# Kernel tuning notes

Hardware: AMD Instinct MI355X
Metric: run time of the kernel (lower is better)

Reference implementation:

```python
import jax, jax.numpy as jnp
import numpy as np

N_FEAT = 27  # 26 embeddings + bot MLP output
LI = np.array([i for i in range(N_FEAT) for j in range(i)])
LJ = np.array([j for i in range(N_FEAT) for j in range(i)])


def _mlp(x, Ws, bs):
    for W, b in zip(Ws, bs):
        x = jax.nn.relu(x @ W + b)
    return x


def setup_inputs() -> dict:
    key = jax.random.key(0)
    ks = jax.random.split(key, 32)
    B, V, D = 32768, 50000, 128
    bot = [13, 512, 256, 128]
    top = [479, 1024, 1024, 512, 256, 1]
    inp = {
        "dense_x": jax.random.normal(ks[0], (B, 13), dtype=jnp.float32),
        "sparse_x": jax.random.randint(ks[1], (B, 26), 0, V, dtype=jnp.int64),
        "emb": jax.random.normal(ks[2], (26, V, D), dtype=jnp.float32) * 0.01,
    }
    for i in range(3):
        inp[f"bw{i}"] = jax.random.normal(ks[3 + i], (bot[i], bot[i + 1]), dtype=jnp.float32) * (1.0 / np.sqrt(bot[i]))
        inp[f"bb{i}"] = jnp.zeros((bot[i + 1],), dtype=jnp.float32)
    for i in range(5):
        inp[f"tw{i}"] = jax.random.normal(ks[8 + i], (top[i], top[i + 1]), dtype=jnp.float32) * (1.0 / np.sqrt(top[i]))
        inp[f"tb{i}"] = jnp.zeros((top[i + 1],), dtype=jnp.float32)
    return inp


def reference(dense_x, sparse_x, emb,
              bw0, bb0, bw1, bb1, bw2, bb2,
              tw0, tb0, tw1, tb1, tw2, tb2, tw3, tb3, tw4, tb4):
    B = dense_x.shape[0]
    bot_out = _mlp(dense_x, [bw0, bw1, bw2], [bb0, bb1, bb2])  # [B, 128]
    # multi-table embedding gather: emb[t, sparse_x[:, t]] -> [B, 26, 128]
    gathered = jnp.take_along_axis(
        emb[None, :, :, :],  # broadcast over batch via vmap-style gather
        sparse_x.T[None, :, :, None].astype(jnp.int32) * 0, 0
    ) if False else jnp.stack(
        [emb[t][sparse_x[:, t]] for t in range(emb.shape[0])], axis=1
    )
    features = jnp.concatenate([bot_out[:, None, :], gathered], axis=1)  # [B, 27, 128]
    # batched dot interaction: [B, 27, 27], then triangular gather
    Z = jnp.einsum('bnd,bmd->bnm', features, features)
    interact = Z[:, LI, LJ]  # [B, 351]
    x = jnp.concatenate([bot_out, interact], axis=1)  # [B, 479]
    return _mlp(x, [tw0, tw1, tw2, tw3, tw4], [tb0, tb1, tb2, tb3, tb4])  # [B, 1]
```

## Files before the change

### kernel.cpp

```cpp
#include <hip/hip_runtime.h>

typedef _Float16 f16;
typedef __attribute__((ext_vector_type(2))) _Float16 f16x2;
typedef __attribute__((ext_vector_type(4))) _Float16 f16x4;
typedef __attribute__((ext_vector_type(8))) _Float16 f16x8;
typedef __attribute__((ext_vector_type(4))) float f32x4;

#define BM 128
#define BN 128
#define BK 32

#define TBM 256
#define TBN 256
#define TBK 64

__device__ __forceinline__ void gl_lds16(const void* g, void* l) {
    __builtin_amdgcn_global_load_lds(
        (const __attribute__((address_space(1))) void*)g,
        (__attribute__((address_space(3))) void*)l, 16, 0, 0);
}

struct ConvtDesc { const float* src; f16* dst; int K, N, Kpad, tileOff; };
struct ConvtArgs { ConvtDesc d[6]; };

__global__ void convt6_kernel(ConvtArgs args)
{
    __shared__ float tile[64][65];
    int bid = blockIdx.x;
    int w = 0;
    #pragma unroll
    for (int i = 1; i < 6; ++i) if (bid >= args.d[i].tileOff) w = i;
    const float* __restrict__ src = args.d[w].src;
    f16* __restrict__ dst = args.d[w].dst;
    int K = args.d[w].K, N = args.d[w].N, Kpad = args.d[w].Kpad;
    int local = bid - args.d[w].tileOff;
    int tk = Kpad >> 6;
    int k0 = (local % tk) * 64;
    int n0 = (local / tk) * 64;
    int tid = threadIdx.x;
    #pragma unroll
    for (int it = 0; it < 16; ++it) {
        int idx = it * 256 + tid;
        int kr = idx >> 6, nc = idx & 63;
        float v = 0.f;
        if (k0 + kr < K) v = src[(size_t)(k0 + kr) * N + n0 + nc];
        tile[kr][nc] = v;
    }
    __syncthreads();
    #pragma unroll
    for (int it = 0; it < 16; ++it) {
        int idx = it * 256 + tid;
        int nr = idx >> 6, kc = idx & 63;
        dst[(size_t)(n0 + nr) * Kpad + k0 + kc] = (f16)tile[kc][nr];
    }
}

__global__ void bot0_kernel(const float* __restrict__ xin, const float* __restrict__ w,
                            const float* __restrict__ bias, f16* __restrict__ out)
{
    int t = blockIdx.x * 256 + threadIdx.x;
    int b = t >> 9, n = t & 511;
    float acc = bias[n];
    #pragma unroll
    for (int k = 0; k < 13; ++k) acc += xin[b * 13 + k] * w[k * 512 + n];
    out[(size_t)b * 512 + n] = (f16)fmaxf(acc, 0.f);
}

__global__ void gemm_f16(const f16* __restrict__ A, const f16* __restrict__ WT,
                         const float* __restrict__ bias, f16* __restrict__ C,
                         int N, int K)
{
    __shared__ __align__(16) f16 lsA[2][BM * BK];
    __shared__ __align__(16) f16 lsB[2][BN * BK];
    int tid  = threadIdx.x;
    int lane = tid & 63;
    int wave = tid >> 6;
    int brow = blockIdx.y * BM;
    int bcol = blockIdx.x * BN;
    int wr = wave >> 1, wc = wave & 1;

    f32x4 acc[4][4] = {};
    int rsel = lane & 15;
    int k8   = lane >> 4;

    auto stage = [&](int buf, int kt) {
        int k0 = kt * BK;
        #pragma unroll
        for (int i = 0; i < 2; ++i) {
            int flat = i * 256 + tid;
            int row  = flat >> 2;
            int slot = flat & 3;
            int sg   = slot ^ ((row >> 1) & 3);
            gl_lds16(A  + (size_t)(brow + row) * K + k0 + sg * 8, lsA[buf] + flat * 8);
            gl_lds16(WT + (size_t)(bcol + row) * K + k0 + sg * 8, lsB[buf] + flat * 8);
        }
    };

    int nK = K / BK;
    stage(0, 0);
    for (int kt = 0; kt < nK; ++kt) {
        int cur = kt & 1;
        if (kt + 1 < nK) {
            stage(cur ^ 1, kt + 1);
            asm volatile("s_waitcnt vmcnt(4)" ::: "memory");
        } else {
            asm volatile("s_waitcnt vmcnt(0)" ::: "memory");
        }
        __builtin_amdgcn_s_barrier();

        __builtin_amdgcn_s_setprio(1);
        f16x8 aF[4], bF[4];
        #pragma unroll
        for (int m = 0; m < 4; ++m) {
            int ra = wr * 64 + m * 16 + rsel;
            int sa = k8 ^ ((ra >> 1) & 3);
            aF[m] = *(const f16x8*)(lsA[cur] + ra * 32 + sa * 8);
        }
        #pragma unroll
        for (int n = 0; n < 4; ++n) {
            int rb = wc * 64 + n * 16 + rsel;
            int sb = k8 ^ ((rb >> 1) & 3);
            bF[n] = *(const f16x8*)(lsB[cur] + rb * 32 + sb * 8);
        }
        #pragma unroll
        for (int m = 0; m < 4; ++m)
            #pragma unroll
            for (int n = 0; n < 4; ++n)
                acc[m][n] = __builtin_amdgcn_mfma_f32_16x16x32_f16(aF[m], bF[n], acc[m][n], 0, 0, 0);
        __builtin_amdgcn_s_setprio(0);
        __builtin_amdgcn_s_barrier();
    }

    #pragma unroll
    for (int n = 0; n < 4; ++n) {
        int col = bcol + wc * 64 + n * 16 + (lane & 15);
        float bv = bias[col];
        #pragma unroll
        for (int m = 0; m < 4; ++m) {
            int rowb = brow + wr * 64 + m * 16 + (lane >> 4) * 4;
            #pragma unroll
            for (int r = 0; r < 4; ++r) {
                float v = acc[m][n][r] + bv;
                C[(size_t)(rowb + r) * N + col] = (f16)fmaxf(v, 0.f);
            }
        }
    }
}

__global__ __launch_bounds__(512, 2) void gemm256_f16(
    const f16* __restrict__ A, const f16* __restrict__ WT,
    const float* __restrict__ bias, f16* __restrict__ C, int N, int K)
{
    __shared__ __align__(16) f16 ls[2][2 * TBM * TBK];
    int tid  = threadIdx.x;
    int lane = tid & 63;
    int wid  = tid >> 6;
    int wm = wid >> 2, wn = wid & 3;

    int nbx = gridDim.x;
    int flat = blockIdx.y * nbx + blockIdx.x;
    int nchunk = (nbx * gridDim.y) >> 3;
    int nf = (flat & 7) * nchunk + (flat >> 3);
    int bx = nf % nbx, by = nf / nbx;
    int brow = by * TBM, bcol = bx * TBN;

    f32x4 acc[8][4] = {};
    int rsel = lane & 15;
    int k8   = lane >> 4;

    const size_t szK = (size_t)K;
    auto stage = [&](int buf, int kt) {
        const f16* gA = A  + (size_t)brow * szK + kt * TBK;
        const f16* gB = WT + (size_t)bcol * szK + kt * TBK;
        f16* dA = &ls[buf][0];
        f16* dB = &ls[buf][TBM * TBK];
        #pragma unroll
        for (int i = 0; i < 4; ++i) {
            int fl  = i * 512 + tid;
            int row = fl >> 3;
            int sl  = fl & 7;
            int sg  = sl ^ (row & 7);
            gl_lds16(gA + (size_t)row * szK + sg * 8, dA + fl * 8);
            gl_lds16(gB + (size_t)row * szK + sg * 8, dB + fl * 8);
        }
    };

    int nK = K / TBK;
    stage(0, 0);
    for (int kt = 0; kt < nK; ++kt) {
        int cur = kt & 1;
        if (kt + 1 < nK) {
            stage(cur ^ 1, kt + 1);
            asm volatile("s_waitcnt vmcnt(8)" ::: "memory");
        } else {
            asm volatile("s_waitcnt vmcnt(0)" ::: "memory");
        }
        __builtin_amdgcn_s_barrier();

        const f16* pA = &ls[cur][0];
        const f16* pB = &ls[cur][TBM * TBK];
        __builtin_amdgcn_s_setprio(1);
        #pragma unroll
        for (int ks = 0; ks < 2; ++ks) {
            f16x8 aF[8], bF[4];
            #pragma unroll
            for (int m = 0; m < 8; ++m) {
                int ra = wm * 128 + m * 16 + rsel;
                int s  = (ks * 4 + k8) ^ (ra & 7);
                aF[m] = *(const f16x8*)(pA + ra * 64 + s * 8);
            }
            #pragma unroll
            for (int n = 0; n < 4; ++n) {
                int rb = wn * 64 + n * 16 + rsel;
                int s  = (ks * 4 + k8) ^ (rb & 7);
                bF[n] = *(const f16x8*)(pB + rb * 64 + s * 8);
            }
            #pragma unroll
            for (int m = 0; m < 8; ++m)
                #pragma unroll
                for (int n = 0; n < 4; ++n)
                    acc[m][n] = __builtin_amdgcn_mfma_f32_16x16x32_f16(aF[m], bF[n], acc[m][n], 0, 0, 0);
        }
        __builtin_amdgcn_s_setprio(0);
        __builtin_amdgcn_s_barrier();
    }

    #pragma unroll
    for (int n = 0; n < 4; ++n) {
        int col = bcol + wn * 64 + n * 16 + (lane & 15);
        float bv = bias[col];
        #pragma unroll
        for (int m = 0; m < 8; ++m) {
            int rowb = brow + wm * 128 + m * 16 + (lane >> 4) * 4;
            #pragma unroll
            for (int r = 0; r < 4; ++r)
                C[(size_t)(rowb + r) * N + col] = (f16)fmaxf(acc[m][n][r] + bv, 0.f);
        }
    }
}

__global__ void interact_mfma(const f16* __restrict__ botout,
                              const float* __restrict__ emb,
                              const int* __restrict__ sparse,
                              f16* __restrict__ x, int V)
{
    __shared__ __align__(16) f16 F[4][32][128];
    __shared__ __align__(16) f16 xs[4][512];
    int tid  = threadIdx.x;
    int lane = tid & 63, wave = tid >> 6;
    int b0 = blockIdx.x * 4;

    for (int t = tid; t < 4 * 27 * 16; t += 256) {
        int s   = t / (27 * 16);
        int rem = t - s * (27 * 16);
        int r   = rem >> 4;
        int c   = rem & 15;
        int b   = b0 + s;
        f16x8 v;
        if (r == 0) {
            v = *(const f16x8*)(botout + (size_t)b * 128 + c * 8);
        } else {
            const float* src = emb + ((size_t)(r - 1) * V + sparse[b * 26 + (r - 1)]) * 128 + c * 8;
            #pragma unroll
            for (int e = 0; e < 8; ++e) v[e] = (f16)src[e];
        }
        *(f16x8*)(&F[s][r][(c ^ (r & 15)) * 8]) = v;
    }
    __syncthreads();

    f32x4 a00 = {}, a10 = {}, a11 = {};
    int rl = lane & 15, ch = lane >> 4;
    #pragma unroll
    for (int ks = 0; ks < 4; ++ks) {
        int c = ks * 4 + ch;
        f16x8 f0 = *(const f16x8*)(&F[wave][rl]     [(c ^ rl) * 8]);
        f16x8 f1 = *(const f16x8*)(&F[wave][16 + rl][(c ^ rl) * 8]);
        a00 = __builtin_amdgcn_mfma_f32_16x16x32_f16(f0, f0, a00, 0, 0, 0);
        a10 = __builtin_amdgcn_mfma_f32_16x16x32_f16(f1, f0, a10, 0, 0, 0);
        a11 = __builtin_amdgcn_mfma_f32_16x16x32_f16(f1, f1, a11, 0, 0, 0);
    }

    #pragma unroll
    for (int r = 0; r < 4; ++r) {
        int i = ch * 4 + r, j = rl;
        if (i > j) xs[wave][128 + (i * (i - 1)) / 2 + j] = (f16)a00[r];
    }
    #pragma unroll
    for (int r = 0; r < 4; ++r) {
        int i = 16 + ch * 4 + r, j = rl;
        if (i < 27) xs[wave][128 + (i * (i - 1)) / 2 + j] = (f16)a10[r];
    }
    #pragma unroll
    for (int r = 0; r < 4; ++r) {
        int i = 16 + ch * 4 + r, j = 16 + rl;
        if (i < 27 && j < i) xs[wave][128 + (i * (i - 1)) / 2 + j] = (f16)a11[r];
    }
    #pragma unroll
    for (int d = lane; d < 128; d += 64) xs[wave][d] = F[wave][0][d];
    if (lane < 33) xs[wave][479 + lane] = (f16)0;
    __syncthreads();

    {
        int b = b0 + wave;
        f16x8 v = *(const f16x8*)(&xs[wave][lane * 8]);
        *(f16x8*)(x + (size_t)b * 512 + lane * 8) = v;
    }
}

__global__ void top4_kernel(const f16* __restrict__ a, const float* __restrict__ w,
                            const float* __restrict__ bias, float* __restrict__ out)
{
    int wave = threadIdx.x >> 6, lane = threadIdx.x & 63;
    int b = blockIdx.x * 4 + wave;
    f16x4 av = *(const f16x4*)(a + (size_t)b * 256 + lane * 4);
    float acc = 0.f;
    #pragma unroll
    for (int k = 0; k < 4; ++k) acc += (float)av[k] * w[lane * 4 + k];
    #pragma unroll
    for (int off = 32; off; off >>= 1) acc += __shfl_xor(acc, off, 64);
    if (lane == 0) out[b] = fmaxf(acc + bias[0], 0.f);
}

extern "C" void kernel_launch(void* const* d_in, const int* in_sizes, int n_in,
                              void* d_out, int out_size, void* d_ws, size_t ws_size,
                              hipStream_t stream)
{
    (void)n_in; (void)out_size; (void)ws_size;
    const float* dense  = (const float*)d_in[0];
    const int*   sparse = (const int*)  d_in[1];
    const float* emb    = (const float*)d_in[2];
    const float* bw0 = (const float*)d_in[3];
    const float* bb0 = (const float*)d_in[4];
    const float* bw1 = (const float*)d_in[5];
    const float* bb1 = (const float*)d_in[6];
    const float* bw2 = (const float*)d_in[7];
    const float* bb2 = (const float*)d_in[8];
    const float* tw0 = (const float*)d_in[9];
    const float* tb0 = (const float*)d_in[10];
    const float* tw1 = (const float*)d_in[11];
    const float* tb1 = (const float*)d_in[12];
    const float* tw2 = (const float*)d_in[13];
    const float* tb2 = (const float*)d_in[14];
    const float* tw3 = (const float*)d_in[15];
    const float* tb3 = (const float*)d_in[16];
    const float* tw4 = (const float*)d_in[17];
    const float* tb4 = (const float*)d_in[18];
    float* out = (float*)d_out;

    const int B = in_sizes[0] / 13;
    const int V = in_sizes[2] / (26 * 128);

    char* ws = (char*)d_ws;
    size_t off = 0;
    auto alloc = [&](size_t bytes) {
        char* p = ws + off;
        off += (bytes + 255) & ~(size_t)255;
        return p;
    };
    f16* S1   = (f16*)alloc((size_t)B * 1024 * 2);
    f16* t1   = (f16*)alloc((size_t)B * 1024 * 2);
    f16* S3   = (f16*)alloc((size_t)B * 512 * 2);
    f16* S4   = (f16*)alloc((size_t)B * 256 * 2);
    f16* act2 = (f16*)alloc((size_t)B * 128 * 2);
    f16* bw1T = (f16*)alloc((size_t)256 * 512 * 2);
    f16* bw2T = (f16*)alloc((size_t)128 * 256 * 2);
    f16* tw0T = (f16*)alloc((size_t)1024 * 512 * 2);
    f16* tw1T = (f16*)alloc((size_t)1024 * 1024 * 2);
    f16* tw2T = (f16*)alloc((size_t)512 * 1024 * 2);
    f16* tw3T = (f16*)alloc((size_t)256 * 512 * 2);
    f16* act0 = S1; f16* t2 = S1;
    f16* x    = S3; f16* t3 = S3;
    f16* act1 = S4; f16* t4 = S4;

    ConvtArgs ca;
    ca.d[0] = { bw1, bw1T,  512,  256,  512,   0 };
    ca.d[1] = { bw2, bw2T,  256,  128,  256,  32 };
    ca.d[2] = { tw0, tw0T,  479, 1024,  512,  40 };
    ca.d[3] = { tw1, tw1T, 1024, 1024, 1024, 168 };
    ca.d[4] = { tw2, tw2T, 1024,  512, 1024, 424 };
    ca.d[5] = { tw3, tw3T,  512,  256,  512, 552 };
    convt6_kernel<<<584, 256, 0, stream>>>(ca);

    bot0_kernel<<<(B * 512) / 256, 256, 0, stream>>>(dense, bw0, bb0, act0);
    gemm_f16<<<dim3( 256/128, B/128), 256, 0, stream>>>(act0, bw1T, bb1, act1,  256,  512);
    gemm_f16<<<dim3( 128/128, B/128), 256, 0, stream>>>(act1, bw2T, bb2, act2,  128,  256);
    interact_mfma<<<B / 4, 256, 0, stream>>>(act2, emb, sparse, x, V);
    gemm256_f16<<<dim3(1024/256, B/256), 512, 0, stream>>>(x,  tw0T, tb0, t1, 1024,  512);
    gemm256_f16<<<dim3(1024/256, B/256), 512, 0, stream>>>(t1, tw1T, tb1, t2, 1024, 1024);
    gemm256_f16<<<dim3( 512/256, B/256), 512, 0, stream>>>(t2, tw2T, tb2, t3,  512, 1024);
    gemm_f16<<<dim3( 256/128, B/128), 256, 0, stream>>>(t3, tw3T, tb3, t4,  256,  512);
    top4_kernel<<<B / 4, 256, 0, stream>>>(t4, tw4, tb4, out);
}
```

Baseline: 407.0 us.

## Split 256x256 GEMM k-step into four quadrant phases with interleaved staging

Replaces the two-stage 256x256 top-MLP GEMM with an 8-phase schedule. Each k-tile is split into four 128x128 quadrant sub-phases. Each sub-phase issues LDS reads, stages one half-tile of the next k-step via global_load_lds, and then runs the MFMAs between barriers. The quadrant order is chosen so A or B fragments are shared between consecutive phases. The aim is to spread global loads across the compute and cut register pressure from fragments, at the cost of more barriers per k-step and hand-tuned vmcnt waits that must stay correct.

Result: no change. 401.0 us (-1.5%).

```diff
diff --git a/kernel.cpp b/kernel.cpp
--- a/kernel.cpp
+++ b/kernel.cpp
@@ -9,10 +9,6 @@
 #define BM 128
 #define BN 128
 #define BK 32
-
-#define TBM 256
-#define TBN 256
-#define TBK 64
 
 __device__ __forceinline__ void gl_lds16(const void* g, void* l) {
     __builtin_amdgcn_global_load_lds(
@@ -147,94 +143,134 @@
     }
 }
 
-__global__ __launch_bounds__(512, 2) void gemm256_f16(
+#define VM(n) asm volatile("s_waitcnt vmcnt(" #n ")" ::: "memory")
+
+#define DSREAD(MH, NH)                                                          \
+    {                                                                           \
+        const f16* pA = ls + cb * 32768 + (MH * 2) * 8192;                      \
+        const f16* pB = ls + cb * 32768 + (NH * 2 + 1) * 8192;                  \
+        _Pragma("unroll")                                                       \
+        for (int m = 0; m < 4; ++m) {                                           \
+            int ra = wmq * 64 + m * 16 + rsel;                                  \
+            _Pragma("unroll")                                                   \
+            for (int ks = 0; ks < 2; ++ks) {                                    \
+                int s = (ks * 4 + k8) ^ (ra & 7);                               \
+                aF[m][ks] = *(const f16x8*)(pA + ra * 64 + s * 8);              \
+            }                                                                   \
+        }                                                                       \
+        _Pragma("unroll")                                                       \
+        for (int n = 0; n < 2; ++n) {                                           \
+            int rb = wnq * 32 + n * 16 + rsel;                                  \
+            _Pragma("unroll")                                                   \
+            for (int ks = 0; ks < 2; ++ks) {                                    \
+                int s = (ks * 4 + k8) ^ (rb & 7);                               \
+                bF[n][ks] = *(const f16x8*)(pB + rb * 64 + s * 8);              \
+            }                                                                   \
+        }                                                                       \
+    }
+
+#define MFMAQ(q)                                                                \
+    __builtin_amdgcn_s_barrier();                                               \
+    asm volatile("s_waitcnt lgkmcnt(0)" ::: "memory");                          \
+    __builtin_amdgcn_sched_barrier(0);                                          \
+    __builtin_amdgcn_s_setprio(1);                                              \
+    _Pragma("unroll")                                                           \
+    for (int m = 0; m < 4; ++m)                                                 \
+        _Pragma("unroll")                                                       \
+        for (int n = 0; n < 2; ++n)                                             \
+            _Pragma("unroll")                                                   \
+            for (int ks = 0; ks < 2; ++ks)                                      \
+                acc[q][m][n] = __builtin_amdgcn_mfma_f32_16x16x32_f16(          \
+                    aF[m][ks], bF[n][ks], acc[q][m][n], 0, 0, 0);               \
+    __builtin_amdgcn_s_setprio(0);                                              \
+    __builtin_amdgcn_s_barrier();
+
+__global__ __launch_bounds__(512, 2) void gemm256_8ph(
     const f16* __restrict__ A, const f16* __restrict__ WT,
     const float* __restrict__ bias, f16* __restrict__ C, int N, int K)
 {
-    __shared__ __align__(16) f16 ls[2][2 * TBM * TBK];
+    __shared__ __align__(16) f16 ls[2 * 4 * 128 * 64];
     int tid  = threadIdx.x;
     int lane = tid & 63;
     int wid  = tid >> 6;
-    int wm = wid >> 2, wn = wid & 3;
+    int wmq = wid >> 2, wnq = wid & 3;
 
     int nbx = gridDim.x;
     int flat = blockIdx.y * nbx + blockIdx.x;
     int nchunk = (nbx * gridDim.y) >> 3;
     int nf = (flat & 7) * nchunk + (flat >> 3);
     int bx = nf % nbx, by = nf / nbx;
-    int brow = by * TBM, bcol = bx * TBN;
-
-    f32x4 acc[8][4] = {};
+    int brow = by * 256, bcol = bx * 256;
+
+    f32x4 acc[4][4][2] = {};
     int rsel = lane & 15;
     int k8   = lane >> 4;
-
     const size_t szK = (size_t)K;
-    auto stage = [&](int buf, int kt) {
-        const f16* gA = A  + (size_t)brow * szK + kt * TBK;
-        const f16* gB = WT + (size_t)bcol * szK + kt * TBK;
-        f16* dA = &ls[buf][0];
-        f16* dB = &ls[buf][TBM * TBK];
-        #pragma unroll
-        for (int i = 0; i < 4; ++i) {
+
+    auto stage_half = [&](int dbuf, int hreg, int kt) {
+        const f16* mat = (hreg & 1) ? WT : A;
+        int base = (hreg & 1) ? bcol : brow;
+        const f16* g = mat + (size_t)(base + (hreg >> 1) * 128) * szK + kt * 64;
+        f16* d = ls + dbuf * 32768 + hreg * 8192;
+        #pragma unroll
+        for (int i = 0; i < 2; ++i) {
             int fl  = i * 512 + tid;
-            int row = fl >> 3;
-            int sl  = fl & 7;
+            int row = fl >> 3, sl = fl & 7;
             int sg  = sl ^ (row & 7);
-            gl_lds16(gA + (size_t)row * szK + sg * 8, dA + fl * 8);
-            gl_lds16(gB + (size_t)row * szK + sg * 8, dB + fl * 8);
+            gl_lds16(g + (size_t)row * szK + sg * 8, d + fl * 8);
         }
     };
 
-    int nK = K / TBK;
-    stage(0, 0);
+    int nK = K / 64;
+    stage_half(0, 0, 0); stage_half(0, 1, 0);
+    stage_half(0, 2, 0); stage_half(0, 3, 0);
+    VM(4);
+    __builtin_amdgcn_s_barrier();
+
     for (int kt = 0; kt < nK; ++kt) {
-        int cur = kt & 1;
-        if (kt + 1 < nK) {
-            stage(cur ^ 1, kt + 1);
-            asm volatile("s_waitcnt vmcnt(8)" ::: "memory");
-        } else {
-            asm volatile("s_waitcnt vmcnt(0)" ::: "memory");
-        }
-        __builtin_amdgcn_s_barrier();
-
-        const f16* pA = &ls[cur][0];
-        const f16* pB = &ls[cur][TBM * TBK];
-        __builtin_amdgcn_s_setprio(1);
-        #pragma unroll
-        for (int ks = 0; ks < 2; ++ks) {
-            f16x8 aF[8], bF[4];
+        int cb = kt & 1, nb = cb ^ 1;
+        bool nl = (kt + 1 < nK);
+        {
+            f16x8 aF[4][2], bF[2][2];
+            DSREAD(0, 0)
+            if (nl) { stage_half(nb, 0, kt + 1); VM(4); } else { VM(2); }
+            MFMAQ(0)
+        }
+        {
+            f16x8 aF[4][2], bF[2][2];
+            DSREAD(1, 0)
+            if (nl) { stage_half(nb, 1, kt + 1); VM(4); } else { VM(0); }
+            MFMAQ(1)
+        }
+        {
+            f16x8 aF[4][2], bF[2][2];
+            DSREAD(1, 1)
+            if (nl) { stage_half(nb, 2, kt + 1); }
+            MFMAQ(2)
+        }
+        {
+            f16x8 aF[4][2], bF[2][2];
+            DSREAD(0, 1)
+            if (nl) { stage_half(nb, 3, kt + 1); VM(4); }
+            MFMAQ(3)
+        }
+    }
+
+    const int mhq[4] = {0, 1, 1, 0};
+    const int nhq[4] = {0, 0, 1, 1};
+    #pragma unroll
+    for (int q = 0; q < 4; ++q) {
+        #pragma unroll
+        for (int n = 0; n < 2; ++n) {
+            int col = bcol + nhq[q] * 128 + wnq * 32 + n * 16 + rsel;
+            float bv = bias[col];
             #pragma unroll
-            for (int m = 0; m < 8; ++m) {
-                int ra = wm * 128 + m * 16 + rsel;
-                int s  = (ks * 4 + k8) ^ (ra & 7);
-                aF[m] = *(const f16x8*)(pA + ra * 64 + s * 8);
+            for (int m = 0; m < 4; ++m) {
+                int rowb = brow + mhq[q] * 128 + wmq * 64 + m * 16 + k8 * 4;
+                #pragma unroll
+                for (int r = 0; r < 4; ++r)
+                    C[(size_t)(rowb + r) * N + col] = (f16)fmaxf(acc[q][m][n][r] + bv, 0.f);
             }
-            #pragma unroll
-            for (int n = 0; n < 4; ++n) {
-                int rb = wn * 64 + n * 16 + rsel;
-                int s  = (ks * 4 + k8) ^ (rb & 7);
-                bF[n] = *(const f16x8*)(pB + rb * 64 + s * 8);
-            }
-            #pragma unroll
-            for (int m = 0; m < 8; ++m)
-                #pragma unroll
-                for (int n = 0; n < 4; ++n)
-                    acc[m][n] = __builtin_amdgcn_mfma_f32_16x16x32_f16(aF[m], bF[n], acc[m][n], 0, 0, 0);
-        }
-        __builtin_amdgcn_s_setprio(0);
-        __builtin_amdgcn_s_barrier();
-    }
-
-    #pragma unroll
-    for (int n = 0; n < 4; ++n) {
-        int col = bcol + wn * 64 + n * 16 + (lane & 15);
-        float bv = bias[col];
-        #pragma unroll
-        for (int m = 0; m < 8; ++m) {
-            int rowb = brow + wm * 128 + m * 16 + (lane >> 4) * 4;
-            #pragma unroll
-            for (int r = 0; r < 4; ++r)
-                C[(size_t)(rowb + r) * N + col] = (f16)fmaxf(acc[m][n][r] + bv, 0.f);
         }
     }
 }
@@ -385,9 +421,9 @@
     gemm_f16<<<dim3( 256/128, B/128), 256, 0, stream>>>(act0, bw1T, bb1, act1,  256,  512);
     gemm_f16<<<dim3( 128/128, B/128), 256, 0, stream>>>(act1, bw2T, bb2, act2,  128,  256);
     interact_mfma<<<B / 4, 256, 0, stream>>>(act2, emb, sparse, x, V);
-    gemm256_f16<<<dim3(1024/256, B/256), 512, 0, stream>>>(x,  tw0T, tb0, t1, 1024,  512);
-    gemm256_f16<<<dim3(1024/256, B/256), 512, 0, stream>>>(t1, tw1T, tb1, t2, 1024, 1024);
-    gemm256_f16<<<dim3( 512/256, B/256), 512, 0, stream>>>(t2, tw2T, tb2, t3,  512, 1024);
+    gemm256_8ph<<<dim3(1024/256, B/256), 512, 0, stream>>>(x,  tw0T, tb0, t1, 1024,  512);
+    gemm256_8ph<<<dim3(1024/256, B/256), 512, 0, stream>>>(t1, tw1T, tb1, t2, 1024, 1024);
+    gemm256_8ph<<<dim3( 512/256, B/256), 512, 0, stream>>>(t2, tw2T, tb2, t3,  512, 1024);
     gemm_f16<<<dim3( 256/128, B/128), 256, 0, stream>>>(t3, tw3T, tb3, t4,  256,  512);
     top4_kernel<<<B / 4, 256, 0, stream>>>(t4, tw4, tb4, out);
 }
```
